# Kernel optimization log

Hardware: AMD Instinct MI355X
Metric: run time of the kernel (lower is better)

Reference implementation:

```python
import jax, jax.numpy as jnp
import numpy as np

B, I, H = 16384, 1024, 1024

def setup_inputs() -> dict:
    key = jax.random.key(0)
    ks = jax.random.split(key, 7)
    scale = 0.02  # small init so gates are not saturated
    return {
        "x": jax.random.normal(ks[0], (B, I), jnp.float32),
        "h_prev": jax.random.normal(ks[1], (B, H), jnp.float32),
        "c_prev": jax.random.normal(ks[2], (B, H), jnp.float32),
        "Wx": jax.random.normal(ks[3], (4, H, I), jnp.float32) * scale,  # order: z,i,f,o
        "bx": jnp.zeros((4, H), jnp.float32),
        "Rh": jax.random.normal(ks[4], (4, H, H), jnp.float32) * scale,
        "bh": jnp.zeros((4, H), jnp.float32),
    }

def reference(x, h_prev, c_prev, Wx, bx, Rh, bh):
    # Fused form of 4 input-GEMMs + 4 recurrent-GEMMs: two einsums over stacked gates.
    # gate order g=0..3 -> z, i, f, o
    pre = (jnp.einsum('bi,ghi->bgh', x, Wx) + bx[None]
           + jnp.einsum('bh,gkh->bgk', h_prev, Rh) + bh[None])  # [B,4,H]
    z = jnp.tanh(pre[:, 0])
    i = jax.nn.sigmoid(pre[:, 1])
    f = jax.nn.sigmoid(pre[:, 2])
    o = jax.nn.sigmoid(pre[:, 3])
    c = f * c_prev + i * z
    h = o * jnp.tanh(c)
    return (h, c)
```

## Files before the change

kernel.cpp:

```cpp
#include <hip/hip_runtime.h>
#include <hip/hip_bf16.h>
#include <stdint.h>


typedef __attribute__((ext_vector_type(8))) short bf16x8;
typedef __attribute__((ext_vector_type(4))) float f32x4;
typedef __attribute__((ext_vector_type(8))) unsigned short u16x8;

#define AS1 __attribute__((address_space(1)))
#define AS3 __attribute__((address_space(3)))

constexpr int BATCH = 16384;
constexpr int HDIM  = 1024;
constexpr int KDIM  = 2048;
constexpr int NDIM  = 4096;

__device__ inline unsigned short f2bf(float f) {
  uint32_t u = __builtin_bit_cast(uint32_t, f);
  u += 0x7fffu + ((u >> 16) & 1u);
  return (unsigned short)(u >> 16);
}
__device__ inline u16x8 cvt8(const float* __restrict__ src) {
  float4 f0 = *(const float4*)src;
  float4 f1 = *(const float4*)(src + 4);
  u16x8 v;
  v[0] = f2bf(f0.x); v[1] = f2bf(f0.y); v[2] = f2bf(f0.z); v[3] = f2bf(f0.w);
  v[4] = f2bf(f1.x); v[5] = f2bf(f1.y); v[6] = f2bf(f1.z); v[7] = f2bf(f1.w);
  return v;
}
__device__ inline float sigmoid_f(float x) {
  float e = __builtin_amdgcn_exp2f(-1.4426950408889634f * x);
  return __builtin_amdgcn_rcpf(1.0f + e);
}
__device__ inline float tanh_f(float x) {
  float e = __builtin_amdgcn_exp2f(2.8853900817779268f * x);
  return 1.0f - 2.0f * __builtin_amdgcn_rcpf(1.0f + e);
}

__global__ void pack_xh(const float* __restrict__ x, const float* __restrict__ hp,
                        unsigned short* __restrict__ xh) {
  const int64_t nch = (int64_t)BATCH * KDIM / 8;
  for (int64_t c = (int64_t)blockIdx.x * blockDim.x + threadIdx.x; c < nch;
       c += (int64_t)gridDim.x * blockDim.x) {
    const int b = (int)(c >> 8);
    const int k = ((int)c & 255) * 8;
    const float* src = (k < 1024) ? (x + (int64_t)b * 1024 + k)
                                  : (hp + (int64_t)b * 1024 + (k - 1024));
    *(u16x8*)(xh + c * 8) = cvt8(src);
  }
}
__global__ void pack_w(const float* __restrict__ Wx, const float* __restrict__ Rh,
                       unsigned short* __restrict__ wp) {
  const int64_t nch = (int64_t)NDIM * KDIM / 8;
  for (int64_t c = (int64_t)blockIdx.x * blockDim.x + threadIdx.x; c < nch;
       c += (int64_t)gridDim.x * blockDim.x) {
    const int np = (int)(c >> 8);
    const int k = ((int)c & 255) * 8;
    const int h = np >> 2, g = np & 3;
    const float* src = (k < 1024) ? (Wx + (int64_t)(g * HDIM + h) * 1024 + k)
                                  : (Rh + (int64_t)(g * HDIM + h) * 1024 + (k - 1024));
    *(u16x8*)(wp + c * 8) = cvt8(src);
  }
}
__global__ void pack_bias(const float* __restrict__ bx, const float* __restrict__ bh,
                          float* __restrict__ bias) {
  int n = blockIdx.x * blockDim.x + threadIdx.x;
  if (n < NDIM) {
    int h = n >> 2, g = n & 3;
    bias[n] = bx[g * HDIM + h] + bh[g * HDIM + h];
  }
}

template <int OFF>
__device__ __forceinline__ bf16x8 dsb128(uint32_t a) {
  bf16x8 r;
  asm volatile("ds_read_b128 %0, %1 offset:%2" : "=v"(r) : "v"(a), "i"(OFF) : "memory");
  return r;
}

#define BARR    asm volatile("s_barrier" ::: "memory")
#define LGKM0   asm volatile("s_waitcnt lgkmcnt(0)" ::: "memory")
#define VM2     asm volatile("s_waitcnt vmcnt(2)" ::: "memory")
#define VM0     asm volatile("s_waitcnt vmcnt(0)" ::: "memory")
#define SCHED0  __builtin_amdgcn_sched_barrier(0)

#define ISS(SLOT) { \
  fa[0] = dsb128<(SLOT)*16384>(av);        fa[1] = dsb128<(SLOT)*16384 + 1024>(av); \
  fa[2] = dsb128<(SLOT)*16384 + 2048>(av); fa[3] = dsb128<(SLOT)*16384 + 3072>(av); \
  fb[0] = dsb128<(SLOT)*16384>(bv);        fb[1] = dsb128<(SLOT)*16384 + 1024>(bv); \
  fb[2] = dsb128<(SLOT)*16384 + 2048>(bv); fb[3] = dsb128<(SLOT)*16384 + 3072>(bv); }

#define MFMA16 { \
  __builtin_amdgcn_s_setprio(1); \
  _Pragma("unroll") for (int mi = 0; mi < 4; ++mi) \
  _Pragma("unroll") for (int ni = 0; ni < 4; ++ni) \
    acc[mi][ni] = __builtin_amdgcn_mfma_f32_16x16x32_bf16(fa[mi], fb[ni], acc[mi][ni], 0, 0, 0); \
  __builtin_amdgcn_s_setprio(0); }

#define STAGE(JS, SLOT) { \
  __builtin_amdgcn_global_load_lds((const AS1 void*)(pA + (int64_t)(JS) * 64), \
      (AS3 void*)(smem_ + (SLOT)*16384 + dstOff), 16, 0, 0); \
  __builtin_amdgcn_global_load_lds((const AS1 void*)(pB + (int64_t)(JS) * 64), \
      (AS3 void*)(smem_ + 65536 + (SLOT)*16384 + dstOff), 16, 0, 0); }

#define BODY(B, SLOT, SLOT2) { \
  BARR; \
  int js = 4 * it + (B) + 2; if (js > 63) js = 63; \
  STAGE(js, SLOT2) \
  ISS(SLOT) \
  LGKM0; SCHED0; \
  MFMA16 \
  VM2; }

__global__ __launch_bounds__(1024, 4) void lstm_gemm(
    const unsigned short* __restrict__ XH, const unsigned short* __restrict__ Wp,
    const float* __restrict__ bias, const float* __restrict__ c_prev,
    float* __restrict__ out_h, float* __restrict__ out_c) {
  __shared__ __align__(1024) char smem_[131072];

  const int tid  = threadIdx.x;
  const int l    = tid & 63;
  const int w    = tid >> 6;
  const int wr   = w >> 2, wc = w & 3;
  const int la   = l & 15;
  const int kg   = l >> 4;

  const int xcd = blockIdx.x & 7;
  const int q   = blockIdx.x >> 3;
  const int tn  = xcd * 2 + (q & 1);
  const int tm  = q >> 1;
  const int m0  = tm * 256;
  const int n0  = tn * 256;

  const int rbase = w * 16 + (l >> 2);
  const int ck    = (l & 3) ^ ((l >> 3) & 3);
  const char* pA = (const char*)XH + (int64_t)(m0 + rbase) * 4096 + ck * 16;
  const char* pB = (const char*)Wp + (int64_t)(n0 + rbase) * 4096 + ck * 16;
  const int dstOff = w * 1024;

  const int cc = kg ^ ((la >> 1) & 3);
  const uint32_t lds0 = (uint32_t)(uintptr_t)(AS3 char*)smem_;
  const uint32_t av = lds0 + wr * 4096 + la * 64 + cc * 16;
  const uint32_t bv = lds0 + 65536 + wc * 4096 + la * 64 + cc * 16;

  f32x4 acc[4][4] = {};
  bf16x8 fa[4], fb[4];

  STAGE(0, 0)
  STAGE(1, 1)
  VM2;

#pragma unroll 1
  for (int it = 0; it < 16; ++it) {
    BODY(0, 0, 2)
    BODY(1, 1, 3)
    BODY(2, 2, 0)
    BODY(3, 3, 1)
  }

  VM0;
  __syncthreads();
  float* ew = (float*)smem_ + w * 1088;
  const float4 bias4 = *(const float4*)(bias + n0 + wc * 64 + 4 * la);
  const int hg = ((n0 + wc * 64) >> 2) + la;

#pragma unroll
  for (int mi = 0; mi < 4; ++mi) {
#pragma unroll
    for (int ni = 0; ni < 4; ++ni)
#pragma unroll
      for (int r = 0; r < 4; ++r)
        ew[(4 * kg + r) * 68 + ni * 16 + la] = acc[mi][ni][r];
#pragma unroll
    for (int p = 0; p < 4; ++p) {
      const int row = p * 4 + kg;
      float4 g4 = *(const float4*)(ew + row * 68 + 4 * la);
      const int b = m0 + wr * 64 + mi * 16 + row;
      const uint32_t oidx = (uint32_t)b * HDIM + (uint32_t)hg;
      const float cp = c_prev[oidx];
      const float zg = tanh_f(g4.x + bias4.x);
      const float ig = sigmoid_f(g4.y + bias4.y);
      const float fg = sigmoid_f(g4.z + bias4.z);
      const float og = sigmoid_f(g4.w + bias4.w);
      const float cn = fg * cp + ig * zg;
      out_h[oidx] = og * tanh_f(cn);
      out_c[oidx] = cn;
    }
  }
}

extern "C" void kernel_launch(void* const* d_in, const int* in_sizes, int n_in,
                              void* d_out, int out_size, void* d_ws, size_t ws_size,
                              hipStream_t stream) {
  const float* x  = (const float*)d_in[0];
  const float* hp = (const float*)d_in[1];
  const float* cp = (const float*)d_in[2];
  const float* Wx = (const float*)d_in[3];
  const float* bx = (const float*)d_in[4];
  const float* Rh = (const float*)d_in[5];
  const float* bh = (const float*)d_in[6];

  unsigned short* XH = (unsigned short*)d_ws;
  unsigned short* Wp = XH + (size_t)BATCH * KDIM;
  float* bias = (float*)(Wp + (size_t)NDIM * KDIM);
  float* out_h = (float*)d_out;
  float* out_c = out_h + (size_t)BATCH * HDIM;

  pack_xh<<<2048, 256, 0, stream>>>(x, hp, XH);
  pack_w<<<1024, 256, 0, stream>>>(Wx, Rh, Wp);
  pack_bias<<<16, 256, 0, stream>>>(bx, bh, bias);
  lstm_gemm<<<1024, 1024, 0, stream>>>(XH, Wp, bias, cp, out_h, out_c);
}
```

Measured before the change: 310.1 us.

## Shrink GEMM tile to 128x128 with 4 waves and merge pack kernels

New measurement: 387.5 us. +25.0%, slower.

```diff
diff --git a/kernel.cpp b/kernel.cpp
--- a/kernel.cpp
+++ b/kernel.cpp
@@ -37,37 +37,39 @@
   return 1.0f - 2.0f * __builtin_amdgcn_rcpf(1.0f + e);
 }
 
-__global__ void pack_xh(const float* __restrict__ x, const float* __restrict__ hp,
-                        unsigned short* __restrict__ xh) {
-  const int64_t nch = (int64_t)BATCH * KDIM / 8;
-  for (int64_t c = (int64_t)blockIdx.x * blockDim.x + threadIdx.x; c < nch;
-       c += (int64_t)gridDim.x * blockDim.x) {
-    const int b = (int)(c >> 8);
-    const int k = ((int)c & 255) * 8;
-    const float* src = (k < 1024) ? (x + (int64_t)b * 1024 + k)
-                                  : (hp + (int64_t)b * 1024 + (k - 1024));
-    *(u16x8*)(xh + c * 8) = cvt8(src);
-  }
-}
-__global__ void pack_w(const float* __restrict__ Wx, const float* __restrict__ Rh,
-                       unsigned short* __restrict__ wp) {
-  const int64_t nch = (int64_t)NDIM * KDIM / 8;
-  for (int64_t c = (int64_t)blockIdx.x * blockDim.x + threadIdx.x; c < nch;
-       c += (int64_t)gridDim.x * blockDim.x) {
-    const int np = (int)(c >> 8);
-    const int k = ((int)c & 255) * 8;
-    const int h = np >> 2, g = np & 3;
-    const float* src = (k < 1024) ? (Wx + (int64_t)(g * HDIM + h) * 1024 + k)
-                                  : (Rh + (int64_t)(g * HDIM + h) * 1024 + (k - 1024));
-    *(u16x8*)(wp + c * 8) = cvt8(src);
-  }
-}
-__global__ void pack_bias(const float* __restrict__ bx, const float* __restrict__ bh,
-                          float* __restrict__ bias) {
-  int n = blockIdx.x * blockDim.x + threadIdx.x;
-  if (n < NDIM) {
-    int h = n >> 2, g = n & 3;
-    bias[n] = bx[g * HDIM + h] + bh[g * HDIM + h];
+__global__ void pack_all(const float* __restrict__ x, const float* __restrict__ hp,
+                         const float* __restrict__ Wx, const float* __restrict__ Rh,
+                         const float* __restrict__ bx, const float* __restrict__ bh,
+                         unsigned short* __restrict__ xh, unsigned short* __restrict__ wp,
+                         float* __restrict__ bias) {
+  const int blk = blockIdx.x;
+  if (blk < 2048) {
+    const int64_t nch = (int64_t)BATCH * KDIM / 8;
+    for (int64_t c = (int64_t)blk * blockDim.x + threadIdx.x; c < nch;
+         c += (int64_t)2048 * blockDim.x) {
+      const int b = (int)(c >> 8);
+      const int k = ((int)c & 255) * 8;
+      const float* src = (k < 1024) ? (x + (int64_t)b * 1024 + k)
+                                    : (hp + (int64_t)b * 1024 + (k - 1024));
+      *(u16x8*)(xh + c * 8) = cvt8(src);
+    }
+  } else {
+    const int wblk = blk - 2048;
+    if (wblk < 16) {
+      const int n = wblk * 256 + threadIdx.x;
+      const int h = n >> 2, g = n & 3;
+      bias[n] = bx[g * HDIM + h] + bh[g * HDIM + h];
+    }
+    const int64_t nch = (int64_t)NDIM * KDIM / 8;
+    for (int64_t c = (int64_t)wblk * blockDim.x + threadIdx.x; c < nch;
+         c += (int64_t)1024 * blockDim.x) {
+      const int np = (int)(c >> 8);
+      const int k = ((int)c & 255) * 8;
+      const int h = np >> 2, g = np & 3;
+      const float* src = (k < 1024) ? (Wx + (int64_t)(g * HDIM + h) * 1024 + k)
+                                    : (Rh + (int64_t)(g * HDIM + h) * 1024 + (k - 1024));
+      *(u16x8*)(wp + c * 8) = cvt8(src);
+    }
   }
 }
 
@@ -80,15 +82,15 @@
 
 #define BARR    asm volatile("s_barrier" ::: "memory")
 #define LGKM0   asm volatile("s_waitcnt lgkmcnt(0)" ::: "memory")
-#define VM2     asm volatile("s_waitcnt vmcnt(2)" ::: "memory")
+#define VM4     asm volatile("s_waitcnt vmcnt(4)" ::: "memory")
 #define VM0     asm volatile("s_waitcnt vmcnt(0)" ::: "memory")
 #define SCHED0  __builtin_amdgcn_sched_barrier(0)
 
 #define ISS(SLOT) { \
-  fa[0] = dsb128<(SLOT)*16384>(av);        fa[1] = dsb128<(SLOT)*16384 + 1024>(av); \
-  fa[2] = dsb128<(SLOT)*16384 + 2048>(av); fa[3] = dsb128<(SLOT)*16384 + 3072>(av); \
-  fb[0] = dsb128<(SLOT)*16384>(bv);        fb[1] = dsb128<(SLOT)*16384 + 1024>(bv); \
-  fb[2] = dsb128<(SLOT)*16384 + 2048>(bv); fb[3] = dsb128<(SLOT)*16384 + 3072>(bv); }
+  fa[0] = dsb128<(SLOT)*8192>(av);        fa[1] = dsb128<(SLOT)*8192 + 1024>(av); \
+  fa[2] = dsb128<(SLOT)*8192 + 2048>(av); fa[3] = dsb128<(SLOT)*8192 + 3072>(av); \
+  fb[0] = dsb128<(SLOT)*8192>(bv);        fb[1] = dsb128<(SLOT)*8192 + 1024>(bv); \
+  fb[2] = dsb128<(SLOT)*8192 + 2048>(bv); fb[3] = dsb128<(SLOT)*8192 + 3072>(bv); }
 
 #define MFMA16 { \
   __builtin_amdgcn_s_setprio(1); \
@@ -99,41 +101,42 @@
 
 #define STAGE(JS, SLOT) { \
   __builtin_amdgcn_global_load_lds((const AS1 void*)(pA + (int64_t)(JS) * 64), \
-      (AS3 void*)(smem_ + (SLOT)*16384 + dstOff), 16, 0, 0); \
+      (AS3 void*)(smem_ + (SLOT)*8192 + dstOff), 16, 0, 0); \
+  __builtin_amdgcn_global_load_lds((const AS1 void*)(pA + 262144 + (int64_t)(JS) * 64), \
+      (AS3 void*)(smem_ + (SLOT)*8192 + 4096 + dstOff), 16, 0, 0); \
   __builtin_amdgcn_global_load_lds((const AS1 void*)(pB + (int64_t)(JS) * 64), \
-      (AS3 void*)(smem_ + 65536 + (SLOT)*16384 + dstOff), 16, 0, 0); }
-
-#define BODY(B, SLOT, SLOT2) { \
-  BARR; \
-  int js = 4 * it + (B) + 2; if (js > 63) js = 63; \
-  STAGE(js, SLOT2) \
-  ISS(SLOT) \
-  LGKM0; SCHED0; \
-  MFMA16 \
-  VM2; }
-
-__global__ __launch_bounds__(1024, 4) void lstm_gemm(
+      (AS3 void*)(smem_ + 32768 + (SLOT)*8192 + dstOff), 16, 0, 0); \
+  __builtin_amdgcn_global_load_lds((const AS1 void*)(pB + 262144 + (int64_t)(JS) * 64), \
+      (AS3 void*)(smem_ + 32768 + (SLOT)*8192 + 4096 + dstOff), 16, 0, 0); }
+
+#define PHASE(P) { \
+  int js = 4 * it + (P) + 2; if (js > 63) js = 63; \
+  STAGE(js, ((P) + 2) & 3) \
+  ISS(P) \
+  LGKM0; SCHED0; MFMA16 VM4; BARR; }
+
+__global__ __launch_bounds__(256, 4) void lstm_gemm(
     const unsigned short* __restrict__ XH, const unsigned short* __restrict__ Wp,
     const float* __restrict__ bias, const float* __restrict__ c_prev,
     float* __restrict__ out_h, float* __restrict__ out_c) {
-  __shared__ __align__(1024) char smem_[131072];
+  __shared__ __align__(1024) char smem_[65536];
 
   const int tid  = threadIdx.x;
   const int l    = tid & 63;
   const int w    = tid >> 6;
-  const int wr   = w >> 2, wc = w & 3;
+  const int wr   = w >> 1, wc = w & 1;
   const int la   = l & 15;
   const int kg   = l >> 4;
 
   const int xcd = blockIdx.x & 7;
   const int q   = blockIdx.x >> 3;
-  const int tn  = xcd * 2 + (q & 1);
-  const int tm  = q >> 1;
-  const int m0  = tm * 256;
-  const int n0  = tn * 256;
-
-  const int rbase = w * 16 + (l >> 2);
-  const int ck    = (l & 3) ^ ((l >> 3) & 3);
+  const int tn  = xcd * 4 + (q & 3);
+  const int tm  = q >> 2;
+  const int m0  = tm * 128;
+  const int n0  = tn * 128;
+
+  const int rbase = tid >> 2;
+  const int ck    = (tid & 3) ^ ((tid >> 3) & 3);
   const char* pA = (const char*)XH + (int64_t)(m0 + rbase) * 4096 + ck * 16;
   const char* pB = (const char*)Wp + (int64_t)(n0 + rbase) * 4096 + ck * 16;
   const int dstOff = w * 1024;
@@ -141,21 +144,21 @@
   const int cc = kg ^ ((la >> 1) & 3);
   const uint32_t lds0 = (uint32_t)(uintptr_t)(AS3 char*)smem_;
   const uint32_t av = lds0 + wr * 4096 + la * 64 + cc * 16;
-  const uint32_t bv = lds0 + 65536 + wc * 4096 + la * 64 + cc * 16;
+  const uint32_t bv = lds0 + 32768 + wc * 4096 + la * 64 + cc * 16;
 
   f32x4 acc[4][4] = {};
   bf16x8 fa[4], fb[4];
 
   STAGE(0, 0)
   STAGE(1, 1)
-  VM2;
+  VM4; BARR;
 
 #pragma unroll 1
   for (int it = 0; it < 16; ++it) {
-    BODY(0, 0, 2)
-    BODY(1, 1, 3)
-    BODY(2, 2, 0)
-    BODY(3, 3, 1)
+    PHASE(0)
+    PHASE(1)
+    PHASE(2)
+    PHASE(3)
   }
 
   VM0;
@@ -206,8 +209,6 @@
   float* out_h = (float*)d_out;
   float* out_c = out_h + (size_t)BATCH * HDIM;
 
-  pack_xh<<<2048, 256, 0, stream>>>(x, hp, XH);
-  pack_w<<<1024, 256, 0, stream>>>(Wx, Rh, Wp);
-  pack_bias<<<16, 256, 0, stream>>>(bx, bh, bias);
-  lstm_gemm<<<1024, 1024, 0, stream>>>(XH, Wp, bias, cp, out_h, out_c);
-}
+  pack_all<<<3072, 256, 0, stream>>>(x, hp, Wx, Rh, bx, bh, XH, Wp, bias);
+  lstm_gemm<<<4096, 256, 0, stream>>>(XH, Wp, bias, cp, out_h, out_c);
+}
```
